# Kernel optimization log

Measured on AMD Instinct MI355X. Metric: run time of the kernel, lower is better.

The kernel has to match this reference:

```python
import jax, jax.numpy as jnp
import numpy as np

B, T, D_MODEL, D_HIDDEN = 4, 8192, 1024, 1024
EPS = 1e-5

def setup_inputs() -> dict:
    key = jax.random.key(0)
    ks = jax.random.split(key, 8)
    s_in = 1.0 / np.sqrt(D_MODEL)
    s_h = 1.0 / np.sqrt(D_HIDDEN)
    return {
        "x": jax.random.normal(ks[0], (B, T, D_MODEL), jnp.float32),
        "W_ih": jax.random.uniform(ks[1], (D_MODEL, D_HIDDEN), jnp.float32, -s_in, s_in),
        "b_ih": jnp.zeros((D_HIDDEN,), jnp.float32),
        "W_gate": jax.random.uniform(ks[2], (D_MODEL, D_HIDDEN), jnp.float32, -s_in, s_in),
        "b_gate": jnp.zeros((D_HIDDEN,), jnp.float32),
        "log_a": jnp.full((D_HIDDEN,), -0.1, jnp.float32),
        "ln_g": jnp.ones((D_HIDDEN,), jnp.float32),
        "ln_b": jnp.zeros((D_HIDDEN,), jnp.float32),
        "W_out": jax.random.uniform(ks[3], (D_HIDDEN, D_HIDDEN), jnp.float32, -s_h, s_h),
        "b_out": jnp.zeros((D_HIDDEN,), jnp.float32),
        "W_proj": jax.random.uniform(ks[4], (D_HIDDEN, D_MODEL), jnp.float32, -s_h, s_h),
        "b_proj": jnp.zeros((D_MODEL,), jnp.float32),
    }

def _scan(alpha, beta):
    # h_t = alpha_t * h_{t-1} + beta_t, h_0 = 0, over axis 1 (time)
    def combine(c1, c2):
        a1, b1 = c1
        a2, b2 = c2
        return a2 * a1, a2 * b1 + b2
    _, h = jax.lax.associative_scan(combine, (alpha, beta), axis=1)
    return h

def reference(x, W_ih, b_ih, W_gate, b_gate, log_a, ln_g, ln_b, W_out, b_out, W_proj, b_proj):
    ih = jnp.einsum("btd,dh->bth", x, W_ih) + b_ih
    gate = jax.nn.sigmoid(jnp.einsum("btd,dh->bth", x, W_gate) + b_gate)
    a = jnp.exp(log_a)  # [H]
    alpha = (1.0 - gate) * a  # [B,T,H]
    beta = gate * ih
    h = _scan(alpha, beta)
    # LayerNorm over last dim
    mu = jnp.mean(h, axis=-1, keepdims=True)
    var = jnp.var(h, axis=-1, keepdims=True)
    hn = (h - mu) * jax.lax.rsqrt(var + EPS) * ln_g + ln_b
    out = jnp.einsum("bth,ho->bto", hn, W_out) + b_out
    return jnp.einsum("bth,hd->btd", out, W_proj) + b_proj
```

## Files before the change

kernel.cpp:

```cpp
#include <hip/hip_runtime.h>

typedef short bhalf8 __attribute__((ext_vector_type(8)));
typedef float floatx4 __attribute__((ext_vector_type(4)));
typedef unsigned short ushortx8 __attribute__((ext_vector_type(8)));

__device__ __forceinline__ unsigned short f2bf(float f){
  union { float f; unsigned int u; } v; v.f = f;
  unsigned int u = v.u;
  u += 0x7fffu + ((u >> 16) & 1u);
  return (unsigned short)(u >> 16);
}
__device__ __forceinline__ float bf2f(unsigned short u){
  union { unsigned int u; float f; } v; v.u = ((unsigned)u) << 16; return v.f;
}
__device__ __forceinline__ unsigned pack2(float a, float b){
  return (unsigned)f2bf(a) | ((unsigned)f2bf(b) << 16);
}

__device__ __forceinline__ void async16(const unsigned short* g, unsigned short* l){
  __builtin_amdgcn_global_load_lds(
      (const __attribute__((address_space(1))) void*)g,
      (__attribute__((address_space(3))) void*)l,
      16, 0, 0);
}

template<int EPI>
__global__ __launch_bounds__(256) void gemm_k(
    const unsigned short* __restrict__ Ab, const unsigned short* __restrict__ BT,
    const float* __restrict__ bias, float* __restrict__ Cf,
    unsigned short* __restrict__ Cb, int K, int ldc)
{
  __shared__ __align__(16) unsigned short As[128*64];
  __shared__ __align__(16) unsigned short Bs[128*64];
  const int tid = threadIdx.x;

  const int nbx = gridDim.x;
  const int nwg = nbx * gridDim.y;
  const int flat = blockIdx.y * nbx + blockIdx.x;
  const int xcd = flat & 7, j = flat >> 3;
  const int q = nwg >> 3, r = nwg & 7;
  const int logical = (xcd < r ? xcd * (q + 1) : r * (q + 1) + (xcd - r) * q) + j;
  const int n0 = (logical % nbx) * 128;
  const int m0 = (logical / nbx) * 128;

  const int wid = tid >> 6, lane = tid & 63;
  const int wr = (wid >> 1) * 64, wc = (wid & 1) * 64;
  const int r16 = lane & 15, quad = lane >> 4;
  const int ldsbase = (tid & ~63) * 8;

  const unsigned short* pA[4];
  const unsigned short* pB[4];
  #pragma unroll
  for (int i = 0; i < 4; ++i) {
    int p = tid + i*256;
    int row = p >> 3;
    int cp = (p & 7) ^ (row & 7);
    pA[i] = Ab + (size_t)(m0+row)*K + cp*8;
    pB[i] = BT + (size_t)(n0+row)*K + cp*8;
  }
  int aoff[2][4], boff[2][4];
  #pragma unroll
  for (int ks = 0; ks < 2; ++ks){
    #pragma unroll
    for (int mi = 0; mi < 4; ++mi){
      int row = wr + mi*16 + r16;
      aoff[ks][mi] = (row*8 + ((ks*4+quad) ^ (row&7))) * 8;
    }
    #pragma unroll
    for (int ni = 0; ni < 4; ++ni){
      int row = wc + ni*16 + r16;
      boff[ks][ni] = (row*8 + ((ks*4+quad) ^ (row&7))) * 8;
    }
  }

  floatx4 acc[4][4];
  #pragma unroll
  for (int i=0;i<4;i++)
    #pragma unroll
    for (int j2=0;j2<4;j2++) acc[i][j2] = {0.f,0.f,0.f,0.f};

  for (int k0 = 0; k0 < K; k0 += 64) {
    #pragma unroll
    for (int i = 0; i < 4; ++i) async16(pA[i], &As[ldsbase + i*2048]);
    #pragma unroll
    for (int i = 0; i < 4; ++i) async16(pB[i], &Bs[ldsbase + i*2048]);
    __syncthreads();
    #pragma unroll
    for (int ks = 0; ks < 2; ++ks) {
      bhalf8 aF[4], bF[4];
      #pragma unroll
      for (int mi=0;mi<4;++mi) aF[mi] = *(const bhalf8*)&As[aoff[ks][mi]];
      #pragma unroll
      for (int ni=0;ni<4;++ni) bF[ni] = *(const bhalf8*)&Bs[boff[ks][ni]];
      #pragma unroll
      for (int mi=0;mi<4;++mi)
        #pragma unroll
        for (int ni=0;ni<4;++ni)
          acc[mi][ni] = __builtin_amdgcn_mfma_f32_16x16x32_bf16(aF[mi], bF[ni], acc[mi][ni], 0, 0, 0);
    }
    __syncthreads();
    #pragma unroll
    for (int i = 0; i < 4; ++i) { pA[i] += 64; pB[i] += 64; }
  }

  #pragma unroll
  for (int mi=0;mi<4;++mi)
    #pragma unroll
    for (int ni=0;ni<4;++ni)
      #pragma unroll
      for (int rr=0;rr<4;++rr){
        int m = m0 + wr + mi*16 + quad*4 + rr;
        int n = n0 + wc + ni*16 + r16;
        float val = acc[mi][ni][rr];
        if (EPI == 0) Cf[(size_t)m*ldc + n] = val;
        else if (EPI == 1) Cf[(size_t)m*ldc + n] = val + bias[n];
        else if (EPI == 3) Cb[(size_t)m*ldc + n] = f2bf(val + bias[n]);
        else Cb[(size_t)n*ldc + m] = f2bf(val);
      }
}

__global__ __launch_bounds__(256) void prep_all(
    const float* __restrict__ W_ih, const float* __restrict__ W_gate,
    const float* __restrict__ W_proj, const float* __restrict__ W_out,
    const float* __restrict__ b_out, const float* __restrict__ b_proj,
    const float* __restrict__ log_a, const float* __restrict__ b_ih,
    const float* __restrict__ b_gate,
    unsigned short* __restrict__ WcatT, unsigned short* __restrict__ WprojT,
    unsigned short* __restrict__ Woutb,
    float* __restrict__ b_comb, float* __restrict__ a_vec, float* __restrict__ bcat)
{
  __shared__ float tile[32][33];
  const int blk = blockIdx.x;
  const int tid = threadIdx.x;
  if (blk < 3072) {
    const int which = blk >> 10;
    const int t = blk & 1023;
    const float* src = (which == 0) ? W_ih : (which == 1) ? W_gate : W_proj;
    unsigned short* dst = (which == 0) ? WcatT : (which == 1) ? (WcatT + 1024*1024) : WprojT;
    const int c0 = (t & 31) * 32, r0 = (t >> 5) * 32;
    const int tx = tid & 31, ty = tid >> 5;
    #pragma unroll
    for (int i = 0; i < 32; i += 8)
      tile[ty+i][tx] = src[(size_t)(r0+ty+i)*1024 + c0+tx];
    __syncthreads();
    #pragma unroll
    for (int i = 0; i < 32; i += 8)
      dst[(size_t)(c0+ty+i)*1024 + r0+tx] = f2bf(tile[tx][ty+i]);
  } else if (blk < 4096) {
    int idx = ((blk - 3072)*256 + tid) * 4;
    float4 v = *(const float4*)(W_out + idx);
    uint2 p;
    p.x = pack2(v.x, v.y);
    p.y = pack2(v.z, v.w);
    *(uint2*)(Woutb + idx) = p;
  } else {
    int d = (blk - 4096)*256 + tid;
    if (d < 1024) {
      float acc = b_proj[d];
      for (int e = 0; e < 1024; ++e)
        acc += b_out[e] * W_proj[(size_t)e*1024 + d];
      b_comb[d] = acc;
      a_vec[d] = __expf(log_a[d]);
      bcat[d] = b_ih[d];
    } else {
      bcat[d] = b_gate[d-1024];
    }
  }
}

__global__ __launch_bounds__(256) void cvt_f32_bf16(const float* __restrict__ src,
                                                    unsigned short* __restrict__ dst)
{
  int idx = (blockIdx.x*256 + threadIdx.x) * 4;
  float4 v = *(const float4*)(src + idx);
  uint2 p;
  p.x = pack2(v.x, v.y);
  p.y = pack2(v.z, v.w);
  *(uint2*)(dst + idx) = p;
}

#define CHUNK 32
#define NCHUNK 256

__device__ __forceinline__ void ab_step(unsigned short iu, unsigned short gu,
                                        float a, float& al, float& be)
{
  float zi = bf2f(iu), zg = bf2f(gu);
  float g = 1.f / (1.f + __expf(-zg));
  al = (1.f - g) * a;
  be = g * zi;
}

__global__ __launch_bounds__(256, 4) void scan_phase1(const unsigned short* __restrict__ pre,
    const float* __restrict__ a_vec, float* __restrict__ Asum, float* __restrict__ Ssum)
{
  int wid = threadIdx.x >> 6, lane = threadIdx.x & 63;
  int u = blockIdx.x*4 + wid;
  int b = u >> 8, c = u & (NCHUNK-1);
  int ch0 = lane*16;
  float a[16], A[16], S[16];
  #pragma unroll
  for (int q=0;q<4;++q) *(float4*)&a[q*4] = *(const float4*)(a_vec + ch0 + q*4);
  #pragma unroll
  for (int j=0;j<16;++j){ A[j]=1.f; S[j]=0.f; }
  size_t base = ((size_t)(b*8192 + c*CHUNK))*2048 + ch0;
  for (int t=0;t<CHUNK;++t){
    ushortx8 i0 = *(const ushortx8*)(pre + base);
    ushortx8 i1 = *(const ushortx8*)(pre + base + 8);
    ushortx8 g0 = *(const ushortx8*)(pre + base + 1024);
    ushortx8 g1 = *(const ushortx8*)(pre + base + 1032);
    #pragma unroll
    for (int j=0;j<8;++j){
      float al, be;
      ab_step(i0[j], g0[j], a[j], al, be);
      A[j] *= al; S[j] = al*S[j] + be;
      ab_step(i1[j], g1[j], a[j+8], al, be);
      A[j+8] *= al; S[j+8] = al*S[j+8] + be;
    }
    base += 2048;
  }
  size_t o = (size_t)u*1024 + ch0;
  #pragma unroll
  for (int q=0;q<4;++q){
    *(float4*)(Asum + o + q*4) = *(const float4*)&A[q*4];
    *(float4*)(Ssum + o + q*4) = *(const float4*)&S[q*4];
  }
}

__global__ __launch_bounds__(256) void scan_phase2(const float* __restrict__ Asum,
    const float* __restrict__ Ssum, float* __restrict__ carry)
{
  int idx = blockIdx.x*256 + threadIdx.x;
  int b = idx >> 10, n = idx & 1023;
  float cur = 0.f;
  size_t o = (size_t)b*NCHUNK*1024 + n;
  for (int c = 0; c < NCHUNK; ++c) {
    carry[o] = cur;
    cur = Asum[o]*cur + Ssum[o];
    o += 1024;
  }
}

__global__ __launch_bounds__(256, 4) void scan_phase3(const unsigned short* __restrict__ pre,
    const float* __restrict__ a_vec, const float* __restrict__ carry,
    const float* __restrict__ ln_g, const float* __restrict__ ln_b,
    unsigned short* __restrict__ hn)
{
  int wid = threadIdx.x >> 6, lane = threadIdx.x & 63;
  int u = blockIdx.x*4 + wid;
  int b = u >> 8, c = u & (NCHUNK-1);
  int ch0 = lane*16;
  float a[16], h[16], g[16], lb[16];
  #pragma unroll
  for (int q=0;q<4;++q){
    *(float4*)&a[q*4]  = *(const float4*)(a_vec + ch0 + q*4);
    *(float4*)&h[q*4]  = *(const float4*)(carry + (size_t)u*1024 + ch0 + q*4);
    *(float4*)&g[q*4]  = *(const float4*)(ln_g + ch0 + q*4);
    *(float4*)&lb[q*4] = *(const float4*)(ln_b + ch0 + q*4);
  }
  size_t base  = ((size_t)(b*8192 + c*CHUNK))*2048 + ch0;
  size_t hbase = ((size_t)(b*8192 + c*CHUNK))*1024 + ch0;
  for (int t=0;t<CHUNK;++t){
    ushortx8 i0 = *(const ushortx8*)(pre + base);
    ushortx8 i1 = *(const ushortx8*)(pre + base + 8);
    ushortx8 g0 = *(const ushortx8*)(pre + base + 1024);
    ushortx8 g1 = *(const ushortx8*)(pre + base + 1032);
    float s = 0.f, s2 = 0.f;
    #pragma unroll
    for (int j=0;j<8;++j){
      float al, be;
      ab_step(i0[j], g0[j], a[j], al, be);
      h[j] = al*h[j] + be;
      s += h[j]; s2 += h[j]*h[j];
      ab_step(i1[j], g1[j], a[j+8], al, be);
      h[j+8] = al*h[j+8] + be;
      s += h[j+8]; s2 += h[j+8]*h[j+8];
    }
    #pragma unroll
    for (int off = 32; off > 0; off >>= 1) {
      s  += __shfl_xor(s,  off);
      s2 += __shfl_xor(s2, off);
    }
    float mu = s * (1.f/1024.f);
    float var = s2 * (1.f/1024.f) - mu*mu;
    float rstd = rsqrtf(var + 1e-5f);
    uint4 o0, o1;
    float v0, v1;
    v0 = (h[0]-mu)*rstd*g[0]+lb[0];  v1 = (h[1]-mu)*rstd*g[1]+lb[1];  o0.x = pack2(v0,v1);
    v0 = (h[2]-mu)*rstd*g[2]+lb[2];  v1 = (h[3]-mu)*rstd*g[3]+lb[3];  o0.y = pack2(v0,v1);
    v0 = (h[4]-mu)*rstd*g[4]+lb[4];  v1 = (h[5]-mu)*rstd*g[5]+lb[5];  o0.z = pack2(v0,v1);
    v0 = (h[6]-mu)*rstd*g[6]+lb[6];  v1 = (h[7]-mu)*rstd*g[7]+lb[7];  o0.w = pack2(v0,v1);
    v0 = (h[8]-mu)*rstd*g[8]+lb[8];  v1 = (h[9]-mu)*rstd*g[9]+lb[9];  o1.x = pack2(v0,v1);
    v0 = (h[10]-mu)*rstd*g[10]+lb[10]; v1 = (h[11]-mu)*rstd*g[11]+lb[11]; o1.y = pack2(v0,v1);
    v0 = (h[12]-mu)*rstd*g[12]+lb[12]; v1 = (h[13]-mu)*rstd*g[13]+lb[13]; o1.z = pack2(v0,v1);
    v0 = (h[14]-mu)*rstd*g[14]+lb[14]; v1 = (h[15]-mu)*rstd*g[15]+lb[15]; o1.w = pack2(v0,v1);
    *(uint4*)(hn + hbase)     = o0;
    *(uint4*)(hn + hbase + 8) = o1;
    base += 2048; hbase += 1024;
  }
}

extern "C" void kernel_launch(void* const* d_in, const int* in_sizes, int n_in,
                              void* d_out, int out_size, void* d_ws, size_t ws_size,
                              hipStream_t stream)
{
  const float* x      = (const float*)d_in[0];
  const float* W_ih   = (const float*)d_in[1];
  const float* b_ih   = (const float*)d_in[2];
  const float* W_gate = (const float*)d_in[3];
  const float* b_gate = (const float*)d_in[4];
  const float* log_a  = (const float*)d_in[5];
  const float* ln_g   = (const float*)d_in[6];
  const float* ln_b   = (const float*)d_in[7];
  const float* W_out  = (const float*)d_in[8];
  const float* b_out  = (const float*)d_in[9];
  const float* W_proj = (const float*)d_in[10];
  const float* b_proj = (const float*)d_in[11];
  float* out = (float*)d_out;

  char* ws = (char*)d_ws;
  size_t off = 0;
  auto alloc = [&](size_t bytes)->char* {
    char* p = ws + off; off += (bytes + 255) & ~(size_t)255; return p;
  };
  unsigned short* pre   = (unsigned short*)alloc((size_t)32768*2048*2);
  unsigned short* hn    = (unsigned short*)alloc((size_t)32768*1024*2);
  unsigned short* xb    = hn;
  unsigned short* WcatT = (unsigned short*)alloc((size_t)2048*1024*2);
  unsigned short* WprojT= (unsigned short*)alloc((size_t)1024*1024*2);
  unsigned short* Woutb = (unsigned short*)alloc((size_t)1024*1024*2);
  unsigned short* WcombT= (unsigned short*)alloc((size_t)1024*1024*2);
  float* Asum           = (float*)alloc((size_t)1024*1024*4);
  float* Ssum           = (float*)alloc((size_t)1024*1024*4);
  float* carry          = (float*)alloc((size_t)1024*1024*4);
  float* b_comb         = (float*)alloc(1024*4);
  float* a_vec          = (float*)alloc(1024*4);
  float* bcat           = (float*)alloc(2048*4);

  prep_all<<<4104, 256, 0, stream>>>(W_ih, W_gate, W_proj, W_out, b_out, b_proj,
                                     log_a, b_ih, b_gate,
                                     WcatT, WprojT, Woutb, b_comb, a_vec, bcat);
  cvt_f32_bf16<<<32768, 256, 0, stream>>>(x, xb);
  gemm_k<2><<<dim3(8,8), 256, 0, stream>>>(Woutb, WprojT, nullptr, nullptr, WcombT, 1024, 1024);
  gemm_k<3><<<dim3(16,256), 256, 0, stream>>>(xb, WcatT, bcat, nullptr, pre, 1024, 2048);
  scan_phase1<<<256, 256, 0, stream>>>(pre, a_vec, Asum, Ssum);
  scan_phase2<<<16, 256, 0, stream>>>(Asum, Ssum, carry);
  scan_phase3<<<256, 256, 0, stream>>>(pre, a_vec, carry, ln_g, ln_b, hn);
  gemm_k<1><<<dim3(8,256), 256, 0, stream>>>(hn, WcombT, b_comb, out, nullptr, 1024, 1024);
}
```

Baseline: 690.3 us.

## Parallelize carry scan with wave shuffles over transposed chunk summaries; drop XCD remap

Phase 1 now stages per-chunk A/S summaries in LDS and writes them transposed, so each channel's 256 chunk summaries are contiguous. Phase 2 changes from a 16-block serial loop over 256 chunks to a 1024-block kernel where each wave runs a 64-lane shuffle scan per channel. This removes a long serial dependency chain and its low occupancy. Phase 3 reads carries with strided scalar loads, and the GEMM drops its XCD-aware tile remapping in favour of plain blockIdx mapping, which may hurt L2 locality.

Measured after the change: 658.3 us. 1.05x faster.

```diff
diff --git a/kernel.cpp b/kernel.cpp
--- a/kernel.cpp
+++ b/kernel.cpp
@@ -33,16 +33,8 @@
   __shared__ __align__(16) unsigned short As[128*64];
   __shared__ __align__(16) unsigned short Bs[128*64];
   const int tid = threadIdx.x;
-
-  const int nbx = gridDim.x;
-  const int nwg = nbx * gridDim.y;
-  const int flat = blockIdx.y * nbx + blockIdx.x;
-  const int xcd = flat & 7, j = flat >> 3;
-  const int q = nwg >> 3, r = nwg & 7;
-  const int logical = (xcd < r ? xcd * (q + 1) : r * (q + 1) + (xcd - r) * q) + j;
-  const int n0 = (logical % nbx) * 128;
-  const int m0 = (logical / nbx) * 128;
-
+  const int n0 = blockIdx.x * 128;
+  const int m0 = blockIdx.y * 128;
   const int wid = tid >> 6, lane = tid & 63;
   const int wr = (wid >> 1) * 64, wc = (wid & 1) * 64;
   const int r16 = lane & 15, quad = lane >> 4;
@@ -192,8 +184,10 @@
 }
 
 __global__ __launch_bounds__(256, 4) void scan_phase1(const unsigned short* __restrict__ pre,
-    const float* __restrict__ a_vec, float* __restrict__ Asum, float* __restrict__ Ssum)
-{
+    const float* __restrict__ a_vec, float* __restrict__ AsT, float* __restrict__ SsT)
+{
+  __shared__ float sA[4][1024];
+  __shared__ float sS[4][1024];
   int wid = threadIdx.x >> 6, lane = threadIdx.x & 63;
   int u = blockIdx.x*4 + wid;
   int b = u >> 8, c = u & (NCHUNK-1);
@@ -219,30 +213,58 @@
     }
     base += 2048;
   }
-  size_t o = (size_t)u*1024 + ch0;
+  #pragma unroll
+  for (int j=0;j<16;++j){ sA[wid][ch0+j] = A[j]; sS[wid][ch0+j] = S[j]; }
+  __syncthreads();
+  const int bb = blockIdx.x >> 6;
+  const int c0 = (blockIdx.x*4) & (NCHUNK-1);
+  const int t = threadIdx.x;
   #pragma unroll
   for (int q=0;q<4;++q){
-    *(float4*)(Asum + o + q*4) = *(const float4*)&A[q*4];
-    *(float4*)(Ssum + o + q*4) = *(const float4*)&S[q*4];
-  }
-}
-
-__global__ __launch_bounds__(256) void scan_phase2(const float* __restrict__ Asum,
-    const float* __restrict__ Ssum, float* __restrict__ carry)
-{
-  int idx = blockIdx.x*256 + threadIdx.x;
-  int b = idx >> 10, n = idx & 1023;
-  float cur = 0.f;
-  size_t o = (size_t)b*NCHUNK*1024 + n;
-  for (int c = 0; c < NCHUNK; ++c) {
-    carry[o] = cur;
-    cur = Asum[o]*cur + Ssum[o];
-    o += 1024;
-  }
+    int ch = t + q*256;
+    float4 va = make_float4(sA[0][ch], sA[1][ch], sA[2][ch], sA[3][ch]);
+    float4 vs = make_float4(sS[0][ch], sS[1][ch], sS[2][ch], sS[3][ch]);
+    size_t o = ((size_t)(bb*1024 + ch))*NCHUNK + c0;
+    *(float4*)(AsT + o) = va;
+    *(float4*)(SsT + o) = vs;
+  }
+}
+
+__global__ __launch_bounds__(256) void scan_phase2(const float* __restrict__ AsT,
+    const float* __restrict__ SsT, float* __restrict__ carryT)
+{
+  int wid = threadIdx.x >> 6, lane = threadIdx.x & 63;
+  int p = blockIdx.x*4 + wid;
+  size_t base = (size_t)p*NCHUNK + lane*4;
+  float4 a4 = *(const float4*)(AsT + base);
+  float4 s4 = *(const float4*)(SsT + base);
+  float A = a4.x, S = s4.x;
+  A = a4.y*A; S = a4.y*S + s4.y;
+  A = a4.z*A; S = a4.z*S + s4.z;
+  A = a4.w*A; S = a4.w*S + s4.w;
+  float iA = A, iS = S;
+  #pragma unroll
+  for (int d = 1; d < 64; d <<= 1) {
+    float pA = __shfl_up(iA, d);
+    float pS = __shfl_up(iS, d);
+    if (lane >= d) { iS = iA*pS + iS; iA = iA*pA; }
+  }
+  float bA = __shfl_up(iA, 1);
+  float bS = __shfl_up(iS, 1);
+  if (lane == 0) { bA = 1.f; bS = 0.f; }
+  float4 c4;
+  c4.x = bS;
+  bS = a4.x*bS + s4.x; bA = a4.x*bA;
+  c4.y = bS;
+  bS = a4.y*bS + s4.y; bA = a4.y*bA;
+  c4.z = bS;
+  bS = a4.z*bS + s4.z;
+  c4.w = bS;
+  *(float4*)(carryT + base) = c4;
 }
 
 __global__ __launch_bounds__(256, 4) void scan_phase3(const unsigned short* __restrict__ pre,
-    const float* __restrict__ a_vec, const float* __restrict__ carry,
+    const float* __restrict__ a_vec, const float* __restrict__ carryT,
     const float* __restrict__ ln_g, const float* __restrict__ ln_b,
     unsigned short* __restrict__ hn)
 {
@@ -254,10 +276,12 @@
   #pragma unroll
   for (int q=0;q<4;++q){
     *(float4*)&a[q*4]  = *(const float4*)(a_vec + ch0 + q*4);
-    *(float4*)&h[q*4]  = *(const float4*)(carry + (size_t)u*1024 + ch0 + q*4);
     *(float4*)&g[q*4]  = *(const float4*)(ln_g + ch0 + q*4);
     *(float4*)&lb[q*4] = *(const float4*)(ln_b + ch0 + q*4);
   }
+  #pragma unroll
+  for (int j=0;j<16;++j)
+    h[j] = carryT[((size_t)b*1024 + ch0 + j)*NCHUNK + c];
   size_t base  = ((size_t)(b*8192 + c*CHUNK))*2048 + ch0;
   size_t hbase = ((size_t)(b*8192 + c*CHUNK))*1024 + ch0;
   for (int t=0;t<CHUNK;++t){
@@ -330,9 +354,9 @@
   unsigned short* WprojT= (unsigned short*)alloc((size_t)1024*1024*2);
   unsigned short* Woutb = (unsigned short*)alloc((size_t)1024*1024*2);
   unsigned short* WcombT= (unsigned short*)alloc((size_t)1024*1024*2);
-  float* Asum           = (float*)alloc((size_t)1024*1024*4);
-  float* Ssum           = (float*)alloc((size_t)1024*1024*4);
-  float* carry          = (float*)alloc((size_t)1024*1024*4);
+  float* AsT            = (float*)alloc((size_t)1024*1024*4);
+  float* SsT            = (float*)alloc((size_t)1024*1024*4);
+  float* carryT         = (float*)alloc((size_t)1024*1024*4);
   float* b_comb         = (float*)alloc(1024*4);
   float* a_vec          = (float*)alloc(1024*4);
   float* bcat           = (float*)alloc(2048*4);
@@ -343,8 +367,8 @@
   cvt_f32_bf16<<<32768, 256, 0, stream>>>(x, xb);
   gemm_k<2><<<dim3(8,8), 256, 0, stream>>>(Woutb, WprojT, nullptr, nullptr, WcombT, 1024, 1024);
   gemm_k<3><<<dim3(16,256), 256, 0, stream>>>(xb, WcatT, bcat, nullptr, pre, 1024, 2048);
-  scan_phase1<<<256, 256, 0, stream>>>(pre, a_vec, Asum, Ssum);
-  scan_phase2<<<16, 256, 0, stream>>>(Asum, Ssum, carry);
-  scan_phase3<<<256, 256, 0, stream>>>(pre, a_vec, carry, ln_g, ln_b, hn);
+  scan_phase1<<<256, 256, 0, stream>>>(pre, a_vec, AsT, SsT);
+  scan_phase2<<<1024, 256, 0, stream>>>(AsT, SsT, carryT);
+  scan_phase3<<<256, 256, 0, stream>>>(pre, a_vec, carryT, ln_g, ln_b, hn);
   gemm_k<1><<<dim3(8,256), 256, 0, stream>>>(hn, WcombT, b_comb, out, nullptr, 1024, 1024);
 }
```
